# Optimization experiments

Measured on AMD Instinct MI355X. Metric: run time of the kernel, lower is better.

## Reference

```python
import jax, jax.numpy as jnp
import numpy as np

N = 1024          # num_rois == nongt_dim
FEAT = 1024       # feat_dim
EMB = 64          # emb_dim
G = 16            # group == fc_dim
DG = FEAT // G    # dim_group = 64
CLS = 80          # coco classes
EPS_POS = 1e-3
EPS_AFF = 1e-6


def setup_inputs() -> dict:
    key = jax.random.key(0)
    ks = jax.random.split(key, 12)
    # valid boxes: xmin,ymin in [0,500), width/height in [1,101)
    xymin = jax.random.uniform(ks[0], (N, 2), dtype=jnp.float32) * 500.0
    wh = 1.0 + jax.random.uniform(ks[1], (N, 2), dtype=jnp.float32) * 100.0
    bbox = jnp.concatenate([xymin[:, :1], xymin[:, 1:], xymin[:, :1] + wh[:, :1], xymin[:, 1:] + wh[:, 1:]], axis=1)
    roi_feat = jax.random.normal(ks[2], (N, FEAT), dtype=jnp.float32)
    s = lambda d: 1.0 / np.sqrt(d)
    return {
        "bbox": bbox,
        "roi_feat": roi_feat,
        "W_pos": jax.random.normal(ks[3], (EMB, G), dtype=jnp.float32) * s(EMB),
        "b_pos": jnp.zeros((G,), jnp.float32),
        "Wq": jax.random.normal(ks[4], (FEAT, FEAT), dtype=jnp.float32) * s(FEAT),
        "bq": jnp.zeros((FEAT,), jnp.float32),
        "Wk": jax.random.normal(ks[5], (FEAT, FEAT), dtype=jnp.float32) * s(FEAT),
        "bk": jnp.zeros((FEAT,), jnp.float32),
        # grouped 1x1 conv: groups=16, in/group=FEAT=1024, out/group=DG=64 -> [G, DG, FEAT]
        "W_conv": jax.random.normal(ks[6], (G, DG, FEAT), dtype=jnp.float32) * s(FEAT),
        "b_conv": jnp.zeros((FEAT,), jnp.float32),
        "W_ro": jax.random.normal(ks[7], (FEAT, CLS), dtype=jnp.float32) * s(FEAT),
        "b_ro": jnp.zeros((CLS,), jnp.float32),
    }


def _position_matrix(bbox):
    xmin, ymin, xmax, ymax = bbox[:, 0], bbox[:, 1], bbox[:, 2], bbox[:, 3]
    w = xmax - xmin + 1.0
    h = ymax - ymin + 1.0
    cx = 0.5 * (xmin + xmax)
    cy = 0.5 * (ymin + ymax)

    def log_clamped(d):
        d = jnp.where(jnp.abs(d) < EPS_POS, EPS_POS, d)
        return jnp.log(jnp.abs(d))

    dx = log_clamped((cx[:, None] - cx[None, :]) / w[:, None])
    dy = log_clamped((cy[:, None] - cy[None, :]) / h[:, None])
    dw = log_clamped(w[:, None] / w[None, :])
    dh = log_clamped(h[:, None] / h[None, :])
    return jnp.stack([dx, dy, dw, dh], axis=2)  # [N, N, 4]


def _position_embedding(pos_mat, feat_dim=EMB, wave_length=1000.0):
    feat_range = jnp.arange(feat_dim // 8, dtype=jnp.float32)          # 8 freqs
    dim_mat = jnp.power(jnp.float32(wave_length), (8.0 / feat_dim) * feat_range)
    div = pos_mat[..., None] / dim_mat                                  # [N, N, 4, 8]
    emb = jnp.concatenate([jnp.sin(div), jnp.cos(div)], axis=-1)        # [N, N, 4, 16]
    return emb.reshape(pos_mat.shape[0], pos_mat.shape[1], feat_dim)    # [N, N, 64]


def reference(bbox, roi_feat, W_pos, b_pos, Wq, bq, Wk, bk, W_conv, b_conv, W_ro, b_ro):
    n = roi_feat.shape[0]
    pos_emb = _position_embedding(_position_matrix(bbox))               # [N, N, 64]
    aff_w = jax.nn.relu(pos_emb @ W_pos + b_pos)                        # [N, N, G]
    aff_w = jnp.transpose(aff_w, (0, 2, 1))                             # [N, G, N]

    q = (roi_feat @ Wq + bq).reshape(n, G, DG)                          # [N, G, DG]
    k = (roi_feat @ Wk + bk).reshape(n, G, DG)
    aff = jnp.einsum('igd,jgd->igj', q, k) * (1.0 / np.sqrt(DG))        # [N, G, N]

    aff_w = jnp.where(aff_w < EPS_AFF, EPS_AFF, aff_w)
    sm = jax.nn.softmax(jnp.log(aff_w) + aff, axis=2)                   # [N, G, N]

    out_t = jnp.einsum('igj,jd->igd', sm, roi_feat)                     # [N, G, FEAT]
    lin = jnp.einsum('igd,gkd->igk', out_t, W_conv).reshape(n, FEAT) + b_conv
    res = roi_feat + lin                                                # [N, FEAT]
    logits = res.sum(axis=0, keepdims=True) @ W_ro + b_ro               # [1, CLS]
    return jax.nn.sigmoid(logits)
```

## Files before the change

kernel.cpp:

```cpp
#include <hip/hip_runtime.h>
#include <hip/hip_bf16.h>
#include <math.h>

#define NN   1024
#define GG   16
#define DGD  64
#define CLS  80
#define SPLIT 4
#define JT_PER 4

typedef __attribute__((ext_vector_type(8))) short short8;
typedef __attribute__((ext_vector_type(4))) float f32x4;
typedef _Float16 half8 __attribute__((ext_vector_type(8)));

__device__ inline void split2t(float x, ushort& h, ushort& l) {
  uint u = __float_as_uint(x);
  h = (ushort)(u >> 16);
  float r = x - __uint_as_float(u & 0xFFFF0000u);
  l = (ushort)(__float_as_uint(r) >> 16);
}

__device__ inline int wslot(int r, int kc) {
  return ((r >> 4) << 6) + ((kc & 3) << 4) + ((r & 15) ^ ((kc & 3) << 2));
}
__device__ inline int rslot(int f, int lane) {
  return (f << 6) + ((lane >> 4) << 4) + ((lane & 15) ^ ((lane >> 4) << 2));
}

__global__ __launch_bounds__(256) void prep_k(
    const float* __restrict__ roi, ushort* __restrict__ roiH, ushort* __restrict__ roiL,
    const float* __restrict__ Wc,  ushort* __restrict__ WcH,  ushort* __restrict__ WcL,
    const float* __restrict__ Wq,  const float* __restrict__ Wk,
    ushort* __restrict__ WqTH, ushort* __restrict__ WqTL,
    ushort* __restrict__ WkTH, ushort* __restrict__ WkTL)
{
  __shared__ float Tl[64][68];
  const int bid = blockIdx.x;
  const int t = threadIdx.x;

  if (bid < 512) {
    const float* src = bid < 256 ? roi : Wc;
    ushort* H = bid < 256 ? roiH : WcH;
    ushort* L = bid < 256 ? roiL : WcL;
    const int base = ((bid & 255) * 256 + t) * 16;
    float v[16];
    *(float4*)&v[0]  = *(const float4*)&src[base];
    *(float4*)&v[4]  = *(const float4*)&src[base + 4];
    *(float4*)&v[8]  = *(const float4*)&src[base + 8];
    *(float4*)&v[12] = *(const float4*)&src[base + 12];
    ushort hs[16], ls[16];
#pragma unroll
    for (int u = 0; u < 16; ++u) split2t(v[u], hs[u], ls[u]);
    *(uint4*)&H[base]     = *(uint4*)&hs[0];
    *(uint4*)&H[base + 8] = *(uint4*)&hs[8];
    *(uint4*)&L[base]     = *(uint4*)&ls[0];
    *(uint4*)&L[base + 8] = *(uint4*)&ls[8];
  } else {
    const int s = bid - 512;
    const float* W = (s >> 8) ? Wk : Wq;
    ushort* H = (s >> 8) ? WkTH : WqTH;
    ushort* L = (s >> 8) ? WkTL : WqTL;
    const int rb = s & 255;
    const int j0 = (rb & 15) * 64, k0 = (rb >> 4) * 64;
    const int r = t >> 2, c = (t & 3) * 16;
#pragma unroll
    for (int u = 0; u < 4; ++u)
      *(float4*)&Tl[r][c + u * 4] = *(const float4*)&W[(k0 + r) * NN + j0 + c + u * 4];
    __syncthreads();
    ushort hs[16], ls[16];
#pragma unroll
    for (int u = 0; u < 16; ++u) split2t(Tl[c + u][r], hs[u], ls[u]);
    const int ob = (j0 + r) * NN + k0 + c;
    *(uint4*)&H[ob]     = *(uint4*)&hs[0];
    *(uint4*)&H[ob + 8] = *(uint4*)&hs[8];
    *(uint4*)&L[ob]     = *(uint4*)&ls[0];
    *(uint4*)&L[ob + 8] = *(uint4*)&ls[8];
  }
}

__global__ __launch_bounds__(256) void fused_m(
    const float* __restrict__ bbox, const float* __restrict__ Wp,
    const float* __restrict__ bp,
    const ushort* __restrict__ roiH, const ushort* __restrict__ roiL,
    const ushort* __restrict__ WqTH, const ushort* __restrict__ WqTL,
    const ushort* __restrict__ WkTH, const ushort* __restrict__ WkTL,
    const ushort* __restrict__ WcH,  const ushort* __restrict__ WcL,
    const float* __restrict__ bq, const float* __restrict__ bk,
    ushort* __restrict__ qHp, ushort* __restrict__ qLp,
    ushort* __restrict__ kHp, ushort* __restrict__ kLp,
    ushort* __restrict__ rwHp, ushort* __restrict__ rwLp,
    float* __restrict__ paff)
{
  __shared__ short8 sAH[256], sAL[256], sBH[512], sBL[512];
  const int bid = blockIdx.x;
  const int t = threadIdx.x, lane = t & 63, w = t >> 6;

  if (bid % 11 < 3) {
    const int gi = (bid / 11) * 3 + (bid % 11);
    const int crow = (lane >> 4) * 4, ccol = lane & 15;
    const int kc = t & 3, r = t >> 2;
    const int sl0 = wslot(r, kc), slB1 = sl0 + 256;
    const int wr = w >> 1, wc = w & 1;

    const ushort *AH_, *AL_, *BH_, *BL_;
    const float* bias;
    ushort *OH_, *OL_;
    int j0;
    if (gi < 256) {
      const int z = gi >> 7, rb = gi & 127;
      const int i0 = (rb >> 3) * 64;
      j0 = (rb & 7) * 128;
      AH_ = roiH + (size_t)i0 * NN;
      AL_ = roiL + (size_t)i0 * NN;
      BH_ = z ? WkTH : WqTH;
      BL_ = z ? WkTL : WqTL;
      bias = z ? bk : bq;
      OH_ = (z ? kHp : qHp) + (size_t)i0 * NN;
      OL_ = (z ? kLp : qLp) + (size_t)i0 * NN;
    } else {
      const int s = gi - 256;
      const int g = s >> 3;
      j0 = (s & 7) * 128;
      AH_ = WcH + (size_t)g * DGD * NN;
      AL_ = WcL + (size_t)g * DGD * NN;
      BH_ = roiH;
      BL_ = roiL;
      bias = nullptr;
      OH_ = rwHp + (size_t)g * DGD * NN;
      OL_ = rwLp + (size_t)g * DGD * NN;
    }

    uint4 vah, val, vbh0, vbh1, vbl0, vbl1;
#define LOADT(kt) { const int ka = (kt) * 32 + (kc << 3); \
    vah  = *(const uint4*)&AH_[(size_t)r * NN + ka]; \
    val  = *(const uint4*)&AL_[(size_t)r * NN + ka]; \
    vbh0 = *(const uint4*)&BH_[(size_t)(j0 + r) * NN + ka]; \
    vbh1 = *(const uint4*)&BH_[(size_t)(j0 + r + 64) * NN + ka]; \
    vbl0 = *(const uint4*)&BL_[(size_t)(j0 + r) * NN + ka]; \
    vbl1 = *(const uint4*)&BL_[(size_t)(j0 + r + 64) * NN + ka]; }

    LOADT(0);
    f32x4 acc[2][4] = {};
    for (int kt = 0; kt < 32; ++kt) {
      __syncthreads();
      *(uint4*)&sAH[sl0] = vah;  *(uint4*)&sAL[sl0] = val;
      *(uint4*)&sBH[sl0] = vbh0; *(uint4*)&sBH[slB1] = vbh1;
      *(uint4*)&sBL[sl0] = vbl0; *(uint4*)&sBL[slB1] = vbl1;
      __syncthreads();
      if (kt + 1 < 32) LOADT(kt + 1);
      short8 ah[2], al[2], bh[4], bl[4];
#pragma unroll
      for (int f = 0; f < 2; ++f) {
        ah[f] = sAH[rslot(wr * 2 + f, lane)];
        al[f] = sAL[rslot(wr * 2 + f, lane)];
      }
#pragma unroll
      for (int f = 0; f < 4; ++f) {
        bh[f] = sBH[rslot(wc * 4 + f, lane)];
        bl[f] = sBL[rslot(wc * 4 + f, lane)];
      }
#pragma unroll
      for (int fm = 0; fm < 2; ++fm)
#pragma unroll
        for (int fn = 0; fn < 4; ++fn) {
          acc[fm][fn] = __builtin_amdgcn_mfma_f32_16x16x32_bf16(ah[fm], bh[fn], acc[fm][fn], 0, 0, 0);
          acc[fm][fn] = __builtin_amdgcn_mfma_f32_16x16x32_bf16(ah[fm], bl[fn], acc[fm][fn], 0, 0, 0);
          acc[fm][fn] = __builtin_amdgcn_mfma_f32_16x16x32_bf16(al[fm], bh[fn], acc[fm][fn], 0, 0, 0);
        }
    }
#undef LOADT
#pragma unroll
    for (int fm = 0; fm < 2; ++fm) {
      const int row = wr * 32 + fm * 16 + crow;
#pragma unroll
      for (int fn = 0; fn < 4; ++fn) {
        const int col = j0 + wc * 64 + fn * 16 + ccol;
        const float bb = bias ? bias[col] : 0.0f;
#pragma unroll
        for (int e = 0; e < 4; ++e) {
          ushort hh, ll; split2t(acc[fm][fn][e] + bb, hh, ll);
          OH_[(size_t)(row + e) * NN + col] = hh;
          OL_[(size_t)(row + e) * NN + col] = ll;
        }
      }
    }
  } else {
    const int i = (bid / 11) * 8 + (bid % 11) - 3;
    half8* sWH = (half8*)sAH;
    half8* sWL = (half8*)sAL;
    float* bpS = (float*)sBH;

    if (t < 128) {
      const int h = t >> 6, kc2 = (t >> 4) & 3, g = t & 15;
      _Float16 hh[8], ll[8];
#pragma unroll
      for (int u = 0; u < 8; ++u) {
        float x = Wp[(h * 32 + kc2 * 8 + u) * 16 + g];
        _Float16 xh = (_Float16)x;
        hh[u] = xh;
        ll[u] = (_Float16)(x - (float)xh);
      }
      sWH[t] = *(half8*)&hh[0];
      sWL[t] = *(half8*)&ll[0];
    }
    if (t < 16) bpS[t] = bp[t];
    __syncthreads();

    const half8 wh0 = sWH[lane], wh1 = sWH[64 + lane];
    const half8 wl0 = sWL[lane], wl1 = sWL[64 + lane];
    const float bb = bpS[lane & 15];

    const float xi0 = bbox[i*4+0], yi0 = bbox[i*4+1], xi1 = bbox[i*4+2], yi1 = bbox[i*4+3];
    const float wi = xi1 - xi0 + 1.0f, hi = yi1 - yi0 + 1.0f;
    const float cxi = 0.5f*(xi0+xi1), cyi = 0.5f*(yi0+yi1);

    const int jr = lane & 15, p = lane >> 4;
    const int csel = p >> 1;
    const float shift = (p & 1) ? 1.5707963267948966f : 0.0f;

    const float invdim[8] = {1.0f, 0.42169650342858224f, 0.17782794100389228f,
        0.07498942093324558f, 0.03162277660168379f, 0.01333521432163324f,
        0.005623413251903491f, 0.0023713737056616554f};

#pragma unroll 1
    for (int f = 0; f < 16; ++f) {
      const int j0 = w * 256 + f * 16;
      float4 bj = *(const float4*)&bbox[(j0 + jr) * 4];
      const float wj = bj.z - bj.x + 1.0f, hj = bj.w - bj.y + 1.0f;
      const float cxj = 0.5f*(bj.x+bj.z), cyj = 0.5f*(bj.y+bj.w);

      const float num1 = csel ? (cyi - cyj) : (cxi - cxj);
      const float den1 = csel ? hi : wi;
      const float pos1 = __logf(fmaxf(fabsf(num1 / den1), 1e-3f));
      const float num2 = csel ? hi : wi;
      const float den2 = csel ? hj : wj;
      const float pos2 = __logf(fmaxf(fabsf(num2 / den2), 1e-3f));

      _Float16 a1[8], a2[8];
#pragma unroll
      for (int u = 0; u < 8; ++u) {
        a1[u] = (_Float16)__sinf(fmaf(pos1, invdim[u], shift));
        a2[u] = (_Float16)__sinf(fmaf(pos2, invdim[u], shift));
      }
      const half8 A1 = *(half8*)&a1[0];
      const half8 A2 = *(half8*)&a2[0];

      f32x4 acc = {0.f, 0.f, 0.f, 0.f};
      acc = __builtin_amdgcn_mfma_f32_16x16x32_f16(A1, wh0, acc, 0, 0, 0);
      acc = __builtin_amdgcn_mfma_f32_16x16x32_f16(A2, wh1, acc, 0, 0, 0);
      acc = __builtin_amdgcn_mfma_f32_16x16x32_f16(A1, wl0, acc, 0, 0, 0);
      acc = __builtin_amdgcn_mfma_f32_16x16x32_f16(A2, wl1, acc, 0, 0, 0);

      float4 ov;
      ov.x = __logf(fmaxf(acc[0] + bb, 1e-6f));
      ov.y = __logf(fmaxf(acc[1] + bb, 1e-6f));
      ov.z = __logf(fmaxf(acc[2] + bb, 1e-6f));
      ov.w = __logf(fmaxf(acc[3] + bb, 1e-6f));
      *(float4*)&paff[((i * GG + (lane & 15)) << 10) + j0 + p * 4] = ov;
    }
  }
}

__global__ __launch_bounds__(256) void attn_m(
    const ushort* __restrict__ qhp, const ushort* __restrict__ qlp,
    const ushort* __restrict__ khp, const ushort* __restrict__ klp,
    const ushort* __restrict__ rwhp, const ushort* __restrict__ rwlp,
    const float* __restrict__ paff,
    float* __restrict__ po, float* __restrict__ pstat)
{
  const int g  = blockIdx.y;
  const int i0 = blockIdx.x * 64;
  const int sp = blockIdx.z;
  const int t  = threadIdx.x;
  const int lane = t & 63, w = t >> 6;

  __shared__ short8 sKH[512], sKL[512], sRH[512], sRL[512];
  __shared__ float PT[4][16][68];

  const int r  = t >> 2;
  const int kc = t & 3;
  const int sl = wslot(r, kc);

  {
    const ushort* s0 = qhp + (size_t)(i0 + r) * NN + g * DGD + kc * 8;
    const ushort* s1 = qlp + (size_t)(i0 + r) * NN + g * DGD + kc * 8;
    *(uint4*)&sKH[sl]       = *(const uint4*)&s0[0];
    *(uint4*)&sKH[sl + 256] = *(const uint4*)&s0[32];
    *(uint4*)&sKL[sl]       = *(const uint4*)&s1[0];
    *(uint4*)&sKL[sl + 256] = *(const uint4*)&s1[32];
  }
  __syncthreads();
  const int qsl = rslot(w, lane);
  const short8 qf_h0 = sKH[qsl], qf_h1 = sKH[256 + qsl];
  const short8 qf_l0 = sKL[qsl], qf_l1 = sKL[256 + qsl];

  const int qr = (lane >> 4) * 4;
  const int qc = lane & 15;

  float m[4], l[4];
  f32x4 o[4] = {};
#pragma unroll
  for (int e = 0; e < 4; ++e) { m[e] = -1e30f; l[e] = 0.f; }

#pragma unroll 1
  for (int jt = sp * JT_PER; jt < sp * JT_PER + JT_PER; ++jt) {
    const int j0 = jt * 64;
    const ushort* ks0 = khp + (size_t)(j0 + r) * NN + g * DGD + kc * 8;
    const ushort* ks1 = klp + (size_t)(j0 + r) * NN + g * DGD + kc * 8;
    uint4 kv00 = *(const uint4*)&ks0[0], kv01 = *(const uint4*)&ks0[32];
    uint4 kv10 = *(const uint4*)&ks1[0], kv11 = *(const uint4*)&ks1[32];
    const ushort* rs0 = rwhp + ((size_t)g * DGD + r) * NN + j0 + kc * 8;
    const ushort* rs1 = rwlp + ((size_t)g * DGD + r) * NN + j0 + kc * 8;
    uint4 rv00 = *(const uint4*)&rs0[0], rv01 = *(const uint4*)&rs0[32];
    uint4 rv10 = *(const uint4*)&rs1[0], rv11 = *(const uint4*)&rs1[32];
    float pf[4][4];
#pragma unroll
    for (int jf = 0; jf < 4; ++jf)
#pragma unroll
      for (int e = 0; e < 4; ++e)
        pf[jf][e] = paff[(((i0 + w * 16 + qr + e) * GG + g) << 10) + j0 + jf * 16 + qc];

    __syncthreads();
    *(uint4*)&sKH[sl] = kv00; *(uint4*)&sKH[sl + 256] = kv01;
    *(uint4*)&sKL[sl] = kv10; *(uint4*)&sKL[sl + 256] = kv11;
    *(uint4*)&sRH[sl] = rv00; *(uint4*)&sRH[sl + 256] = rv01;
    *(uint4*)&sRL[sl] = rv10; *(uint4*)&sRL[sl + 256] = rv11;
    __syncthreads();

    f32x4 s4[4];
#pragma unroll
    for (int jf = 0; jf < 4; ++jf) {
      const int bs = rslot(jf, lane);
      short8 bh0 = sKH[bs], bh1 = sKH[256 + bs];
      short8 bl0 = sKL[bs], bl1 = sKL[256 + bs];
      f32x4 a = {0.f, 0.f, 0.f, 0.f};
      a = __builtin_amdgcn_mfma_f32_16x16x32_bf16(qf_h0, bh0, a, 0, 0, 0);
      a = __builtin_amdgcn_mfma_f32_16x16x32_bf16(qf_h1, bh1, a, 0, 0, 0);
      a = __builtin_amdgcn_mfma_f32_16x16x32_bf16(qf_h0, bl0, a, 0, 0, 0);
      a = __builtin_amdgcn_mfma_f32_16x16x32_bf16(qf_h1, bl1, a, 0, 0, 0);
      a = __builtin_amdgcn_mfma_f32_16x16x32_bf16(qf_l0, bh0, a, 0, 0, 0);
      a = __builtin_amdgcn_mfma_f32_16x16x32_bf16(qf_l1, bh1, a, 0, 0, 0);
      s4[jf] = a;
    }

#pragma unroll
    for (int e = 0; e < 4; ++e) {
      float v0 = fmaf(s4[0][e], 0.125f, pf[0][e]);
      float v1 = fmaf(s4[1][e], 0.125f, pf[1][e]);
      float v2 = fmaf(s4[2][e], 0.125f, pf[2][e]);
      float v3 = fmaf(s4[3][e], 0.125f, pf[3][e]);
      float tm = fmaxf(fmaxf(v0, v1), fmaxf(v2, v3));
#pragma unroll
      for (int off = 1; off < 16; off <<= 1) tm = fmaxf(tm, __shfl_xor(tm, off, 64));
      const float mn = fmaxf(m[e], tm);
      const float sc = __expf(m[e] - mn);
      v0 = __expf(v0 - mn); v1 = __expf(v1 - mn);
      v2 = __expf(v2 - mn); v3 = __expf(v3 - mn);
      float ts = (v0 + v1) + (v2 + v3);
#pragma unroll
      for (int off = 1; off < 16; off <<= 1) ts += __shfl_xor(ts, off, 64);
      l[e] = l[e] * sc + ts;
      m[e] = mn;
#pragma unroll
      for (int nf = 0; nf < 4; ++nf) o[nf][e] *= sc;
      PT[w][qr + e][ 0 + qc] = v0;
      PT[w][qr + e][16 + qc] = v1;
      PT[w][qr + e][32 + qc] = v2;
      PT[w][qr + e][48 + qc] = v3;
    }

    short8 ph[2], pl[2];
#pragma unroll
    for (int h = 0; h < 2; ++h) {
      const float* psrc = &PT[w][lane & 15][h * 32 + (lane >> 4) * 8];
      float4 x = *(const float4*)&psrc[0];
      float4 y = *(const float4*)&psrc[4];
      float vv[8] = {x.x, x.y, x.z, x.w, y.x, y.y, y.z, y.w};
      ushort hh[8], ll[8];
#pragma unroll
      for (int u = 0; u < 8; ++u) split2t(vv[u], hh[u], ll[u]);
      ph[h] = *(short8*)&hh[0];
      pl[h] = *(short8*)&ll[0];
    }

#pragma unroll
    for (int nf = 0; nf < 4; ++nf) {
      const int bs = rslot(nf, lane);
      short8 rh0 = sRH[bs], rh1 = sRH[256 + bs];
      short8 rl0 = sRL[bs], rl1 = sRL[256 + bs];
      f32x4 a = o[nf];
      a = __builtin_amdgcn_mfma_f32_16x16x32_bf16(ph[0], rh0, a, 0, 0, 0);
      a = __builtin_amdgcn_mfma_f32_16x16x32_bf16(ph[1], rh1, a, 0, 0, 0);
      a = __builtin_amdgcn_mfma_f32_16x16x32_bf16(ph[0], rl0, a, 0, 0, 0);
      a = __builtin_amdgcn_mfma_f32_16x16x32_bf16(ph[1], rl1, a, 0, 0, 0);
      a = __builtin_amdgcn_mfma_f32_16x16x32_bf16(pl[0], rh0, a, 0, 0, 0);
      a = __builtin_amdgcn_mfma_f32_16x16x32_bf16(pl[1], rh1, a, 0, 0, 0);
      o[nf] = a;
    }
  }

  const size_t idx = ((size_t)blockIdx.x * GG + g) * SPLIT + sp;
  float* pot = po + idx * 4096;
#pragma unroll
  for (int nf = 0; nf < 4; ++nf)
#pragma unroll
    for (int e = 0; e < 4; ++e)
      pot[(w * 16 + qr + e) * 64 + nf * 16 + qc] = o[nf][e];
  if (qc == 0) {
#pragma unroll
    for (int e = 0; e < 4; ++e) {
      const int row = w * 16 + qr + e;
      pstat[(idx * 64 + row) * 2]     = m[e];
      pstat[(idx * 64 + row) * 2 + 1] = l[e];
    }
  }
}

__global__ __launch_bounds__(256) void combine_k(
    const float* __restrict__ po, const float* __restrict__ pstat,
    const float* __restrict__ roi, const float* __restrict__ bconv,
    float* __restrict__ res)
{
  const int it = blockIdx.x, g = blockIdx.y;
  const int t = threadIdx.x;
  const int row = t >> 2, c0 = (t & 3) * 16;
  const size_t base = ((size_t)it * GG + g) * SPLIT;

  float ms[SPLIT], ls[SPLIT];
#pragma unroll
  for (int s = 0; s < SPLIT; ++s) {
    float2 st = *(const float2*)&pstat[((base + s) * 64 + row) * 2];
    ms[s] = st.x; ls[s] = st.y;
  }
  float M = ms[0];
#pragma unroll
  for (int s = 1; s < SPLIT; ++s) M = fmaxf(M, ms[s]);
  float wgt[SPLIT], L = 0.f;
#pragma unroll
  for (int s = 0; s < SPLIT; ++s) { wgt[s] = __expf(ms[s] - M); L = fmaf(ls[s], wgt[s], L); }
  const float rL = 1.0f / L;

  const int grow = it * 64 + row;
  const int f0   = g * DGD + c0;
#pragma unroll
  for (int c = 0; c < 4; ++c) {
    float4 acc = {0.f, 0.f, 0.f, 0.f};
#pragma unroll
    for (int s = 0; s < SPLIT; ++s) {
      float4 v = *(const float4*)&po[(base + s) * 4096 + row * 64 + c0 + c * 4];
      acc.x = fmaf(v.x, wgt[s], acc.x);
      acc.y = fmaf(v.y, wgt[s], acc.y);
      acc.z = fmaf(v.z, wgt[s], acc.z);
      acc.w = fmaf(v.w, wgt[s], acc.w);
    }
    float4 r4 = *(const float4*)&roi[grow * NN + f0 + c * 4];
    float4 b4 = *(const float4*)&bconv[f0 + c * 4];
    float4 ov;
    ov.x = r4.x + b4.x + acc.x * rL;
    ov.y = r4.y + b4.y + acc.y * rL;
    ov.z = r4.z + b4.z + acc.z * rL;
    ov.w = r4.w + b4.w + acc.w * rL;
    *(float4*)&res[grow * NN + f0 + c * 4] = ov;
  }
}

__global__ __launch_bounds__(256) void colsum_partial_k(
    const float* __restrict__ res, float* __restrict__ part)
{
  const int d  = blockIdx.x * 256 + threadIdx.x;
  const int r0 = blockIdx.y * 128;
  float s0 = 0.f, s1 = 0.f, s2 = 0.f, s3 = 0.f;
  for (int i = 0; i < 128; i += 4) {
    s0 += res[(r0 + i    ) * NN + d];
    s1 += res[(r0 + i + 1) * NN + d];
    s2 += res[(r0 + i + 2) * NN + d];
    s3 += res[(r0 + i + 3) * NN + d];
  }
  part[blockIdx.y * NN + d] = (s0 + s1) + (s2 + s3);
}

__global__ __launch_bounds__(640) void final_k(
    const float* __restrict__ part, const float* __restrict__ W_ro,
    const float* __restrict__ b_ro, float* __restrict__ out)
{
  __shared__ float cs[1024];
  __shared__ float red[8][CLS];
  const int t = threadIdx.x;

  for (int u = t; u < 1024; u += 640) {
    float s = 0.f;
#pragma unroll
    for (int p = 0; p < 8; ++p) s += part[p * NN + u];
    cs[u] = s;
  }
  __syncthreads();

  {
    const int c = t % CLS, s = t / CLS;
    float acc = 0.f;
    const int d0 = s * 128;
#pragma unroll 8
    for (int d = d0; d < d0 + 128; ++d)
      acc = fmaf(cs[d], W_ro[d * CLS + c], acc);
    red[s][c] = acc;
  }
  __syncthreads();

  if (t < CLS) {
    float lg = b_ro[t];
#pragma unroll
    for (int s = 0; s < 8; ++s) lg += red[s][t];
    out[t] = 1.0f / (1.0f + __expf(-lg));
  }
}

extern "C" void kernel_launch(void* const* d_in, const int* in_sizes, int n_in,
                              void* d_out, int out_size, void* d_ws, size_t ws_size,
                              hipStream_t stream) {
  const float* bbox  = (const float*)d_in[0];
  const float* roi   = (const float*)d_in[1];
  const float* W_pos = (const float*)d_in[2];
  const float* b_pos = (const float*)d_in[3];
  const float* Wq    = (const float*)d_in[4];
  const float* bq    = (const float*)d_in[5];
  const float* Wk    = (const float*)d_in[6];
  const float* bk    = (const float*)d_in[7];
  const float* Wc    = (const float*)d_in[8];
  const float* bcv   = (const float*)d_in[9];
  const float* W_ro  = (const float*)d_in[10];
  const float* b_ro  = (const float*)d_in[11];

  float* ws = (float*)d_ws;
  float* paff = ws;
  ushort* roiH = (ushort*)(ws + (16 << 20));
  ushort* roiL = (ushort*)(ws + (16 << 20) + (1 << 19));
  ushort* WqTH = (ushort*)(ws + (17 << 20));
  ushort* WqTL = (ushort*)(ws + (17 << 20) + (1 << 19));
  ushort* WkTH = (ushort*)(ws + (18 << 20));
  ushort* WkTL = (ushort*)(ws + (18 << 20) + (1 << 19));
  ushort* WcH  = (ushort*)(ws + (19 << 20));
  ushort* WcL  = (ushort*)(ws + (19 << 20) + (1 << 19));
  ushort* qHp  = (ushort*)(ws + (20 << 20));
  ushort* qLp  = (ushort*)(ws + (20 << 20) + (1 << 19));
  ushort* kHp  = (ushort*)(ws + (21 << 20));
  ushort* kLp  = (ushort*)(ws + (21 << 20) + (1 << 19));
  ushort* rwHp = (ushort*)(ws + (22 << 20));
  ushort* rwLp = (ushort*)(ws + (22 << 20) + (1 << 19));
  float* po    = ws + (16 << 20);
  float* pstat = ws + (23 << 20);
  float* part  = ws + (23 << 20) + (1 << 18);
  float* res   = ws + (23 << 20) + (1 << 19);

  prep_k<<<1024, 256, 0, stream>>>(roi, roiH, roiL, Wc, WcH, WcL,
                                   Wq, Wk, WqTH, WqTL, WkTH, WkTL);

  fused_m<<<1408, 256, 0, stream>>>(bbox, W_pos, b_pos,
                                    roiH, roiL, WqTH, WqTL, WkTH, WkTL,
                                    WcH, WcL, bq, bk,
                                    qHp, qLp, kHp, kLp, rwHp, rwLp, paff);

  attn_m<<<dim3(16, 16, SPLIT), 256, 0, stream>>>(qHp, qLp, kHp, kLp, rwHp, rwLp,
                                                  paff, po, pstat);
  combine_k<<<dim3(16, 16), 256, 0, stream>>>(po, pstat, roi, bcv, res);
  colsum_partial_k<<<dim3(4, 8), 256, 0, stream>>>(res, part);
  final_k<<<1, 640, 0, stream>>>(part, W_ro, b_ro, (float*)d_out);
}
```

Before: 127.5 us.

## Fuse column sum into combine kernel and approximate low-frequency sin/cos with polynomials

Removes the separate colsum_partial kernel. The combine kernel now reduces its output columns through shared-memory atomics and then global atomics into a buffer that is zeroed by a memset beforehand. Separately, the four lowest-frequency position-embedding terms use truncated Taylor polynomials for sin/cos instead of __sinf. This cuts one launch and a re-read of res, at the cost of atomic contention, a nondeterministic summation order, and a less accurate approximation when the argument is large (|pos|*invdim can reach about 0.2).

Result: slower. 131.1 us (+2.8%).

```diff
diff --git a/kernel.cpp b/kernel.cpp
--- a/kernel.cpp
+++ b/kernel.cpp
@@ -216,7 +216,8 @@
 
     const int jr = lane & 15, p = lane >> 4;
     const int csel = p >> 1;
-    const float shift = (p & 1) ? 1.5707963267948966f : 0.0f;
+    const bool iscos = (p & 1);
+    const float shift = iscos ? 1.5707963267948966f : 0.0f;
 
     const float invdim[8] = {1.0f, 0.42169650342858224f, 0.17782794100389228f,
         0.07498942093324558f, 0.03162277660168379f, 0.01333521432163324f,
@@ -238,9 +239,21 @@
 
       _Float16 a1[8], a2[8];
 #pragma unroll
-      for (int u = 0; u < 8; ++u) {
+      for (int u = 0; u < 4; ++u) {
         a1[u] = (_Float16)__sinf(fmaf(pos1, invdim[u], shift));
         a2[u] = (_Float16)__sinf(fmaf(pos2, invdim[u], shift));
+      }
+#pragma unroll
+      for (int u = 4; u < 8; ++u) {
+        const float b1 = pos1 * invdim[u];
+        const float b2 = pos2 * invdim[u];
+        const float q1 = b1 * b1, q2 = b2 * b2;
+        const float s1 = b1 * fmaf(q1, -0.16666667f, 1.0f);
+        const float c1 = fmaf(q1, -0.5f, 1.0f);
+        const float s2 = b2 * fmaf(q2, -0.16666667f, 1.0f);
+        const float c2 = fmaf(q2, -0.5f, 1.0f);
+        a1[u] = (_Float16)(iscos ? c1 : s1);
+        a2[u] = (_Float16)(iscos ? c2 : s2);
       }
       const half8 A1 = *(half8*)&a1[0];
       const half8 A2 = *(half8*)&a2[0];
@@ -419,12 +432,16 @@
 __global__ __launch_bounds__(256) void combine_k(
     const float* __restrict__ po, const float* __restrict__ pstat,
     const float* __restrict__ roi, const float* __restrict__ bconv,
-    float* __restrict__ res)
+    float* __restrict__ res, float* __restrict__ colsum)
 {
+  __shared__ float cls[64];
   const int it = blockIdx.x, g = blockIdx.y;
   const int t = threadIdx.x;
   const int row = t >> 2, c0 = (t & 3) * 16;
   const size_t base = ((size_t)it * GG + g) * SPLIT;
+
+  if (t < 64) cls[t] = 0.f;
+  __syncthreads();
 
   float ms[SPLIT], ls[SPLIT];
 #pragma unroll
@@ -461,38 +478,25 @@
     ov.z = r4.z + b4.z + acc.z * rL;
     ov.w = r4.w + b4.w + acc.w * rL;
     *(float4*)&res[grow * NN + f0 + c * 4] = ov;
-  }
-}
-
-__global__ __launch_bounds__(256) void colsum_partial_k(
-    const float* __restrict__ res, float* __restrict__ part)
-{
-  const int d  = blockIdx.x * 256 + threadIdx.x;
-  const int r0 = blockIdx.y * 128;
-  float s0 = 0.f, s1 = 0.f, s2 = 0.f, s3 = 0.f;
-  for (int i = 0; i < 128; i += 4) {
-    s0 += res[(r0 + i    ) * NN + d];
-    s1 += res[(r0 + i + 1) * NN + d];
-    s2 += res[(r0 + i + 2) * NN + d];
-    s3 += res[(r0 + i + 3) * NN + d];
-  }
-  part[blockIdx.y * NN + d] = (s0 + s1) + (s2 + s3);
+    const int lc = c0 + c * 4;
+    atomicAdd(&cls[lc + 0], ov.x);
+    atomicAdd(&cls[lc + 1], ov.y);
+    atomicAdd(&cls[lc + 2], ov.z);
+    atomicAdd(&cls[lc + 3], ov.w);
+  }
+  __syncthreads();
+  if (t < 64) atomicAdd(&colsum[g * DGD + t], cls[t]);
 }
 
 __global__ __launch_bounds__(640) void final_k(
-    const float* __restrict__ part, const float* __restrict__ W_ro,
+    const float* __restrict__ colsum, const float* __restrict__ W_ro,
     const float* __restrict__ b_ro, float* __restrict__ out)
 {
   __shared__ float cs[1024];
   __shared__ float red[8][CLS];
   const int t = threadIdx.x;
 
-  for (int u = t; u < 1024; u += 640) {
-    float s = 0.f;
-#pragma unroll
-    for (int p = 0; p < 8; ++p) s += part[p * NN + u];
-    cs[u] = s;
-  }
+  for (int u = t; u < 1024; u += 640) cs[u] = colsum[u];
   __syncthreads();
 
   {
@@ -546,10 +550,12 @@
   ushort* kLp  = (ushort*)(ws + (21 << 20) + (1 << 19));
   ushort* rwHp = (ushort*)(ws + (22 << 20));
   ushort* rwLp = (ushort*)(ws + (22 << 20) + (1 << 19));
-  float* po    = ws + (16 << 20);
-  float* pstat = ws + (23 << 20);
-  float* part  = ws + (23 << 20) + (1 << 18);
-  float* res   = ws + (23 << 20) + (1 << 19);
+  float* po     = ws + (16 << 20);
+  float* pstat  = ws + (23 << 20);
+  float* colsum = ws + (23 << 20) + (1 << 18);
+  float* res    = ws + (23 << 20) + (1 << 19);
+
+  hipMemsetAsync((void*)colsum, 0, 1024 * sizeof(float), stream);
 
   prep_k<<<1024, 256, 0, stream>>>(roi, roiH, roiL, Wc, WcH, WcL,
                                    Wq, Wk, WqTH, WqTL, WkTH, WkTL);
@@ -561,7 +567,6 @@
 
   attn_m<<<dim3(16, 16, SPLIT), 256, 0, stream>>>(qHp, qLp, kHp, kLp, rwHp, rwLp,
                                                   paff, po, pstat);
-  combine_k<<<dim3(16, 16), 256, 0, stream>>>(po, pstat, roi, bcv, res);
-  colsum_partial_k<<<dim3(4, 8), 256, 0, stream>>>(res, part);
-  final_k<<<1, 640, 0, stream>>>(part, W_ro, b_ro, (float*)d_out);
-}
+  combine_k<<<dim3(16, 16), 256, 0, stream>>>(po, pstat, roi, bcv, res, colsum);
+  final_k<<<1, 640, 0, stream>>>(colsum, W_ro, b_ro, (float*)d_out);
+}
```
